# Kernel tuning notes

Measured on AMD Instinct MI355X. Metric: run time of the kernel, lower is better.

Reference implementation:

```python
import jax, jax.numpy as jnp
import numpy as np

EPS = 1e-5

def conv1x1(x, w, b):
    # x: [B,C,H,W], w: [O,C], b: [O]
    return jnp.einsum('bchw,oc->bohw', x, w) + b[None, :, None, None]

def bn_eval(x, g, b, m, v):
    scale = g / jnp.sqrt(v + EPS)
    return x * scale[None, :, None, None] + (b - m * scale)[None, :, None, None]

def setup_inputs() -> dict:
    key = jax.random.key(0)
    ks = jax.random.split(key, 32)
    B, Ch, Cl, H, W = 8, 256, 128, 64, 64
    r = Cl // 2
    red = 16  # CBAM channel-attention reduction
    s = 0.05
    n = lambda k, shape: jax.random.normal(k, shape, dtype=jnp.float32) * s
    inp = {
        'x': jax.random.normal(ks[0], (B, Ch, H, W), dtype=jnp.float32),
        'x0': jax.random.normal(ks[1], (B, Cl, H, W), dtype=jnp.float32),
        # CNL (flag=0)
        'cnl_g_w': n(ks[2], (Cl, Cl)), 'cnl_g_b': n(ks[3], (Cl,)),
        'cnl_theta_w': n(ks[4], (Cl, Ch)), 'cnl_theta_b': n(ks[5], (Cl,)),
        'cnl_phi_w': n(ks[6], (Cl, Cl)), 'cnl_phi_b': n(ks[7], (Cl,)),
        'cnl_W_w': n(ks[8], (Ch, Cl)), 'cnl_W_b': n(ks[9], (Ch,)),
        'cnl_bn_g': n(ks[10], (Ch,)), 'cnl_bn_b': n(ks[11], (Ch,)),
        'cnl_bn_m': n(ks[12], (Ch,)),
        'cnl_bn_v': jax.random.uniform(ks[13], (Ch,), dtype=jnp.float32) + 0.5,
        # PNL (reduc_ratio=2)
        'pnl_g_w': n(ks[14], (r, Cl)), 'pnl_g_b': n(ks[15], (r,)),
        'pnl_theta_w': n(ks[16], (r, Ch)), 'pnl_theta_b': n(ks[17], (r,)),
        'pnl_phi_w': n(ks[18], (r, Cl)), 'pnl_phi_b': n(ks[19], (r,)),
        'pnl_W_w': n(ks[20], (Ch, r)), 'pnl_W_b': n(ks[21], (Ch,)),
        'pnl_bn_g': n(ks[22], (Ch,)), 'pnl_bn_b': n(ks[23], (Ch,)),
        'pnl_bn_m': n(ks[24], (Ch,)),
        'pnl_bn_v': jax.random.uniform(ks[25], (Ch,), dtype=jnp.float32) + 0.5,
        # CBAM
        'ca_fc1_w': n(ks[26], (Ch // red, Ch)),
        'ca_fc2_w': n(ks[27], (Ch, Ch // red)),
        'sa_conv_w': n(ks[28], (1, 2, 7, 7)),
        'fusion_weight': jnp.float32(0.5),
    }
    return inp

def mdfo_forward(x, x0, cnl_g_w, cnl_g_b, cnl_theta_w, cnl_theta_b, cnl_phi_w, cnl_phi_b,
                 cnl_W_w, cnl_W_b, cnl_bn_g, cnl_bn_b, cnl_bn_m, cnl_bn_v,
                 pnl_g_w, pnl_g_b, pnl_theta_w, pnl_theta_b, pnl_phi_w, pnl_phi_b,
                 pnl_W_w, pnl_W_b, pnl_bn_g, pnl_bn_b, pnl_bn_m, pnl_bn_v,
                 ca_fc1_w, ca_fc2_w, sa_conv_w, fusion_weight):
    B, Ch, H, W = x.shape
    Cl = x0.shape[1]
    N = H * W
    # ---- CNL (flag=0): channel-space affinity [B, Cl, Cl] ----
    g_x = conv1x1(x0, cnl_g_w, cnl_g_b).reshape(B, Cl, N)
    th = conv1x1(x, cnl_theta_w, cnl_theta_b).reshape(B, Cl, N)
    ph = conv1x1(x0, cnl_phi_w, cnl_phi_b).reshape(B, Cl, N)
    att = jnp.einsum('bcn,bdn->bcd', th, ph) / Cl  # energy / energy.size(-1)
    y = jnp.einsum('bcd,bdn->bcn', att, g_x).reshape(B, Cl, H, W)
    z_cnl = bn_eval(conv1x1(y, cnl_W_w, cnl_W_b), cnl_bn_g, cnl_bn_b, cnl_bn_m, cnl_bn_v) + x
    # ---- PNL: pixel-space affinity [B, N/2, N/2] (faithful channel-folding reshape) ----
    r = Cl // 2
    M = N // 2
    g2 = conv1x1(x0, pnl_g_w, pnl_g_b).reshape(B, Cl, M).transpose(0, 2, 1)          # [B,M,Cl]
    t2 = conv1x1(z_cnl, pnl_theta_w, pnl_theta_b).reshape(B, Cl, M).transpose(0, 2, 1)
    p2 = conv1x1(x0, pnl_phi_w, pnl_phi_b).reshape(B, Cl, M)
    att2 = jnp.einsum('bnc,bcm->bnm', t2, p2) / M
    y2 = jnp.einsum('bnm,bmc->bnc', att2, g2).transpose(0, 2, 1).reshape(B, r, H, W)
    z_pnl = bn_eval(conv1x1(y2, pnl_W_w, pnl_W_b), pnl_bn_g, pnl_bn_b, pnl_bn_m, pnl_bn_v) + z_cnl
    # ---- CBAM: channel attention then spatial attention ----
    def mlp(v):
        return jnp.einsum('bh,oh->bo', jax.nn.relu(jnp.einsum('bc,hc->bh', v, ca_fc1_w)), ca_fc2_w)
    ca = jax.nn.sigmoid(mlp(z_pnl.mean(axis=(2, 3))) + mlp(z_pnl.max(axis=(2, 3))))
    xc = z_pnl * ca[:, :, None, None]
    sa_in = jnp.concatenate([xc.mean(axis=1, keepdims=True), xc.max(axis=1, keepdims=True)], axis=1)
    sa = jax.lax.conv_general_dilated(sa_in, sa_conv_w, (1, 1), ((3, 3), (3, 3)),
                                      dimension_numbers=('NCHW', 'OIHW', 'NCHW'))
    z_cbam = xc * jax.nn.sigmoid(sa)
    # ---- weighted fusion (dropout is identity in eval mode) ----
    return fusion_weight * z_cbam + (1.0 - fusion_weight) * x

def reference(x, x0, cnl_g_w, cnl_g_b, cnl_theta_w, cnl_theta_b, cnl_phi_w, cnl_phi_b,
              cnl_W_w, cnl_W_b, cnl_bn_g, cnl_bn_b, cnl_bn_m, cnl_bn_v,
              pnl_g_w, pnl_g_b, pnl_theta_w, pnl_theta_b, pnl_phi_w, pnl_phi_b,
              pnl_W_w, pnl_W_b, pnl_bn_g, pnl_bn_b, pnl_bn_m, pnl_bn_v,
              ca_fc1_w, ca_fc2_w, sa_conv_w, fusion_weight):
    return mdfo_forward(x, x0, cnl_g_w, cnl_g_b, cnl_theta_w, cnl_theta_b, cnl_phi_w, cnl_phi_b,
                        cnl_W_w, cnl_W_b, cnl_bn_g, cnl_bn_b, cnl_bn_m, cnl_bn_v,
                        pnl_g_w, pnl_g_b, pnl_theta_w, pnl_theta_b, pnl_phi_w, pnl_phi_b,
                        pnl_W_w, pnl_W_b, pnl_bn_g, pnl_bn_b, pnl_bn_m, pnl_bn_v,
                        ca_fc1_w, ca_fc2_w, sa_conv_w, fusion_weight)
```

## Files before the change

kernel.cpp:

```cpp
#include <hip/hip_runtime.h>
#include <math.h>

typedef unsigned short u16;
typedef unsigned int   u32;
typedef __bf16 bf16_8 __attribute__((ext_vector_type(8)));
typedef float  f32x4  __attribute__((ext_vector_type(4)));

constexpr int CH   = 256;
constexpr int NPIX = 4096;

__device__ __forceinline__ u16 f2bf(float f) {
    u32 u = __float_as_uint(f);
    u = (u + 0x7FFFu + ((u >> 16) & 1u)) >> 16;
    return (u16)u;
}
__device__ __forceinline__ float bf2f(u16 h) { return __uint_as_float((u32)h << 16); }
__device__ __forceinline__ u32 encF(float f) {
    u32 u = __float_as_uint(f);
    return u ^ (u32)(((int)u >> 31) | 0x80000000);
}
__device__ __forceinline__ float decF(u32 u) {
    return __uint_as_float((u >> 31) ? (u ^ 0x80000000u) : ~u);
}

struct GJob {
    const u16* A; const u16* B;
    u16* outB; float* outF; u32* maxOut;
    const float* bias; const float* bng; const float* bnb; const float* bnm;
    const float* bnv; const u16* resB;
    long long sA, sB, sC, sR;
    int lda, ldb, ldc, K, nSplit, mode, biasRow, gx, gy, nBlk;
};
struct GJobs { GJob j[4]; int n; };

template<int BN>
__global__ __launch_bounds__(256, 2)
void mfma_multi(GJobs jobs)
{
    constexpr int BM = 64, BK = 64;
    constexpr int WN = BN / 4;
    constexpr int NT = WN / 16;
    __shared__ __align__(16) u16 smem[BM * BK + BN * BK];
    u16* As = smem;
    u16* Bs = smem + BM * BK;
    u16* Ct = smem;
    float* sSum = (float*)&smem[BM * BN];
    u32*   sMax = (u32*)&smem[BM * BN + 512];

    int ji = 0, start = 0;
    {
        int bxx = blockIdx.x;
        while (ji + 1 < jobs.n && bxx >= start + jobs.j[ji].nBlk) {
            start += jobs.j[ji].nBlk; ++ji;
        }
    }
    const GJob J = jobs.j[ji];
    const int local = blockIdx.x - start;
    const int per = J.gx * J.gy;
    const int bz = local / per;
    const int r2 = local - bz * per;
    const int by = r2 / J.gx;
    const int bx2 = r2 - by * J.gx;
// ... 76 lines not shown
        int lc = wave * WN + nt * 16 + lm;
#pragma unroll
        for (int mt = 0; mt < 4; ++mt)
#pragma unroll
            for (int r = 0; r < 4; ++r)
                Ct[(mt * 16 + q * 4 + r) * BN + lc] = f2bf(acc[mt][nt][r]);
    }
    __syncthreads();

    constexpr int CPR = BN / 8;
    constexpr int RSTEP = 256 / CPR;
    constexpr int PT = BM / RSTEP;
    const int cc = (tid % CPR) * 8;
    const int lr0 = tid / CPR;

    float csc[8], csh[8], cbv[8];
    if (J.mode == 4 || J.mode == 5) {
#pragma unroll
        for (int j = 0; j < 8; ++j) {
            int C = nBase + cc + j;
            float sc = J.bng[C] * rsqrtf(J.bnv[C] + 1e-5f);
            csc[j] = sc;
            csh[j] = J.bnb[C] - J.bnm[C] * sc;
            cbv[j] = J.bias[C];
        }
    } else if (J.mode == 0 && J.bias && !J.biasRow) {
#pragma unroll
        for (int j = 0; j < 8; ++j) cbv[j] = J.bias[nBase + cc + j];
    } else {
#pragma unroll
        for (int j = 0; j < 8; ++j) cbv[j] = 0.f;
    }

    float tsum[8], tmax[8];
#pragma unroll
    for (int j = 0; j < 8; ++j) { tsum[j] = 0.f; tmax[j] = -1e30f; }

#pragma unroll
    for (int i = 0; i < PT; ++i) {
        int lr = lr0 + i * RSTEP;
        int R = mBase + lr;
        uint4 raw = *(const uint4*)&Ct[lr * BN + cc];
        u32 w[4] = {raw.x, raw.y, raw.z, raw.w};
        float v[8];
#pragma unroll
        for (int jj = 0; jj < 4; ++jj) {
            v[2 * jj]     = bf2f((u16)(w[jj] & 0xFFFFu));
            v[2 * jj + 1] = bf2f((u16)(w[jj] >> 16));
        }
        if (J.mode == 0) {
            float rb = (J.bias && J.biasRow) ? J.bias[R] : 0.f;
            u32 o[4];
#pragma unroll
            for (int jj = 0; jj < 4; ++jj) {
                u16 lo = f2bf(v[2 * jj] + cbv[2 * jj] + rb);
                u16 hi = f2bf(v[2 * jj + 1] + cbv[2 * jj + 1] + rb);
                o[jj] = (u32)lo | ((u32)hi << 16);
            }
            *(uint4*)&J.outB[(size_t)batch * J.sC + (size_t)R * J.ldc + nBase + cc] =
                make_uint4(o[0], o[1], o[2], o[3]);
        } else if (J.mode == 3) {
            u16 ev[4], od[4];
#pragma unroll
            for (int jj = 0; jj < 4; ++jj) {
                ev[jj] = f2bf(v[2 * jj]);
                od[jj] = f2bf(v[2 * jj + 1]);
            }
            int c0 = (cc >> 1);
            u32 e0 = (u32)ev[0] | ((u32)ev[1] << 16), e1 = (u32)ev[2] | ((u32)ev[3] << 16);
            u32 d0 = (u32)od[0] | ((u32)od[1] << 16), d1 = (u32)od[2] | ((u32)od[3] << 16);
            *(uint2*)&J.outB[(size_t)batch * J.sC + (size_t)R * 64 + c0] = make_uint2(e0, e1);
            *(uint2*)&J.outB[(size_t)batch * J.sC + (size_t)(R + 2048) * 64 + c0] = make_uint2(d0, d1);
        } else {
            size_t off = (size_t)batch * J.sC + (size_t)R * J.ldc + nBase + cc;
            uint4 rr = *(const uint4*)&J.resB[(size_t)batch * J.sR + (size_t)R * J.ldc + nBase + cc];
            u32 rw[4] = {rr.x, rr.y, rr.z, rr.w};
            u32 o[4];
#pragma unroll
            for (int jj = 0; jj < 4; ++jj) {
                float z0 = (v[2 * jj] + cbv[2 * jj]) * csc[2 * jj] + csh[2 * jj] +
                           bf2f((u16)(rw[jj] & 0xFFFFu));
                float z1 = (v[2 * jj + 1] + cbv[2 * jj + 1]) * csc[2 * jj + 1] +
                           csh[2 * jj + 1] + bf2f((u16)(rw[jj] >> 16));
                u16 lo = f2bf(z0), hi = f2bf(z1);
                o[jj] = (u32)lo | ((u32)hi << 16);
                tsum[2 * jj] += bf2f(lo); tsum[2 * jj + 1] += bf2f(hi);
                tmax[2 * jj] = fmaxf(tmax[2 * jj], bf2f(lo));
                tmax[2 * jj + 1] = fmaxf(tmax[2 * jj + 1], bf2f(hi));
            }
            *(uint4*)&J.outB[off] = make_uint4(o[0], o[1], o[2], o[3]);
        }
    }

    if (J.mode == 5) {
        sSum[tid] = 0.f; sMax[tid] = 0u;
        __syncthreads();
#pragma unroll
        for (int j = 0; j < 8; ++j) {
            atomicAdd(&sSum[cc + j], tsum[j]);
            atomicMax(&sMax[cc + j], encF(tmax[j]));
        }
        __syncthreads();
        atomicAdd(&J.outF[batch * CH + tid], sSum[tid]);
        atomicMax(&J.maxOut[batch * CH + tid], sMax[tid]);
    }
}

__global__ __launch_bounds__(256, 2)
void zcnl_t2(const u16* __restrict__ yTg, const u16* __restrict__ w_z,
             const u16* __restrict__ xTb, const u16* __restrict__ w_t2,
             u16* __restrict__ zb, u16* __restrict__ T2f,
             const float* __restrict__ bias,
             const float* __restrict__ bng, const float* __restrict__ bnb,
             const float* __restrict__ bnm, const float* __restrict__ bnv,
             const float* __restrict__ bias2)
{
    constexpr int BM = 64, BK = 64, BN = 256, WN = 64, NT = 4;
    constexpr int LDP = 264;
    __shared__ __align__(16) u16 smem[33792];
    u16* As = smem;
    u16* Bs = smem + 4096;
    u16* Ct = smem;
    u16* B2 = smem + 16896;

    const int batch = blockIdx.z;
    const int mBase = blockIdx.y * BM;
    const int tid = threadIdx.x;
    const int wave = tid >> 6, lane = tid & 63, lm = lane & 15, q = lane >> 4;
    const u16* Ab = yTg + (size_t)batch * 524288;

    f32x4 acc[4][NT];
#pragma unroll
    for (int i = 0; i < 4; ++i)
#pragma unroll
        for (int j = 0; j < NT; ++j) acc[i][j] = f32x4{0.f, 0.f, 0.f, 0.f};

    const int srow = tid >> 3, sc8 = tid & 7;
    for (int k0 = 0; k0 < 128; k0 += BK) {
        __syncthreads();
#pragma unroll
        for (int it = 0; it < 2; ++it) {
            int r = srow + it * 32;
            uint4 v = *(const uint4*)(Ab + (size_t)(mBase + r) * 128 + k0 + sc8 * 8);
            *(uint4*)&As[r * BK + ((sc8 ^ (r & 7)) * 8)] = v;
        }
#pragma unroll
        for (int it = 0; it < 8; ++it) {
            int r = srow + it * 32;
            uint4 v = *(const uint4*)(w_z + (size_t)r * 128 + k0 + sc8 * 8);
            *(uint4*)&Bs[r * BK + ((sc8 ^ (r & 7)) * 8)] = v;
        }
        __syncthreads();
#pragma unroll
        for (int ks = 0; ks < 2; ++ks) {
            bf16_8 af[4], bfr[NT];
#pragma unroll
            for (int mt = 0; mt < 4; ++mt) {
                int r = mt * 16 + lm;
                af[mt] = *(const bf16_8*)&As[r * BK + (((ks * 4 + q) ^ (lm & 7)) * 8)];
            }
#pragma unroll
            for (int nt = 0; nt < NT; ++nt) {
                int r = wave * WN + nt * 16 + lm;
                bfr[nt] = *(const bf16_8*)&Bs[r * BK + (((ks * 4 + q) ^ (lm & 7)) * 8)];
            }
#pragma unroll
            for (int mt = 0; mt < 4; ++mt)
#pragma unroll
                for (int nt = 0; nt < NT; ++nt)
                    acc[mt][nt] = __builtin_amdgcn_mfma_f32_16x16x32_bf16(
                        af[mt], bfr[nt], acc[mt][nt], 0, 0, 0);
        }
    }

    __syncthreads();
#pragma unroll
    for (int nt = 0; nt < NT; ++nt) {
        int lc = wave * WN + nt * 16 + lm;
#pragma unroll
        for (int mt = 0; mt < 4; ++mt)
#pragma unroll
            for (int r = 0; r < 4; ++r)
                Ct[(mt * 16 + q * 4 + r) * LDP + lc] = f2bf(acc[mt][nt][r]);
    }
#pragma unroll
    for (int i = 0; i < 8; ++i) {
        int id = tid + i * 256;
        int r = id >> 5, ch = id & 31;
        *(uint4*)&B2[r * LDP + ch * 8] = *(const uint4*)(w_t2 + r * 256 + ch * 8);
    }
    __syncthreads();

    const int cc = (tid & 31) * 8;
    const int lr0 = tid >> 5;
    float csc[8], csh[8], cbv[8];
#pragma unroll
    for (int j = 0; j < 8; ++j) {
        int C = cc + j;
        float sc = bng[C] * rsqrtf(bnv[C] + 1e-5f);
        csc[j] = sc;
        csh[j] = bnb[C] - bnm[C] * sc;
        cbv[j] = bias[C];
    }
#pragma unroll
    for (int i = 0; i < 8; ++i) {
        int lr = lr0 + i * 8;
        int R = mBase + lr;
        uint4 raw = *(const uint4*)&Ct[lr * LDP + cc];
        u32 w[4] = {raw.x, raw.y, raw.z, raw.w};
        uint4 rr = *(const uint4*)&xTb[(size_t)batch * 1048576 + (size_t)R * 256 + cc];
        u32 rw[4] = {rr.x, rr.y, rr.z, rr.w};
        u32 o[4];
#pragma unroll
        for (int jj = 0; jj < 4; ++jj) {
            float z0 = (bf2f((u16)(w[jj] & 0xFFFFu)) + cbv[2 * jj]) * csc[2 * jj] +
                       csh[2 * jj] + bf2f((u16)(rw[jj] & 0xFFFFu));
            float z1 = (bf2f((u16)(w[jj] >> 16)) + cbv[2 * jj + 1]) * csc[2 * jj + 1] +
                       csh[2 * jj + 1] + bf2f((u16)(rw[jj] >> 16));
            o[jj] = (u32)f2bf(z0) | ((u32)f2bf(z1) << 16);
        }
        *(uint4*)&zb[(size_t)batch * 1048576 + (size_t)R * 256 + cc] =
            make_uint4(o[0], o[1], o[2], o[3]);
        *(uint4*)&Ct[lr * LDP + cc] = make_uint4(o[0], o[1], o[2], o[3]);
    }
    __syncthreads();

    f32x4 acc2[4];
#pragma unroll
    for (int i = 0; i < 4; ++i) acc2[i] = f32x4{0.f, 0.f, 0.f, 0.f};
#pragma unroll
    for (int ks = 0; ks < 8; ++ks) {
        bf16_8 bf = *(const bf16_8*)&B2[(wave * 16 + lm) * LDP + ks * 32 + q * 8];
#pragma unroll
        for (int mt = 0; mt < 4; ++mt) {
            bf16_8 af = *(const bf16_8*)&Ct[(mt * 16 + lm) * LDP + ks * 32 + q * 8];
            acc2[mt] = __builtin_amdgcn_mfma_f32_16x16x32_bf16(af, bf, acc2[mt], 0, 0, 0);
        }
    }
    const int d = wave * 16 + lm;
    const float b2v = bias2[d];
#pragma unroll
    for (int mt = 0; mt < 4; ++mt)
#pragma unroll
        for (int r = 0; r < 4; ++r) {
            int pix = mBase + mt * 16 + q * 4 + r;
            T2f[(size_t)batch * 262144 + (size_t)(pix & 2047) * 128 + (pix >> 11) * 64 + d] =
                f2bf(acc2[mt][r] + b2v);
        }
}

__global__ __launch_bounds__(256)
void prep_tcast(const float* __restrict__ x, u16* __restrict__ xTb,
                const float* __restrict__ x0, u16* __restrict__ x0Tb,
                const float* w0, const float* w1, const float* w2, const float* w3,
                const float* w4, const float* w5, const float* w6, const float* w7,
                const float* pgb, const float* ppb,
                float* __restrict__ zr, u16* __restrict__ wsb, float* __restrict__ pb128)
{
    __shared__ u16 T[64][68];
    const int bx = blockIdx.x, tid = threadIdx.x;
    if (bx < 3072) {
        const int b = bx / 384, rem = bx % 384;
        const int by = rem / 64, nb = (rem % 64) * 64;
// ... 28 lines not shown
            if      (j < 32768)  v = w0[j];
            else if (j < 49152)  v = w1[j - 32768];
            else if (j < 65536)  v = w2[j - 49152];
            else if (j < 98304)  v = w3[j - 65536];
            else if (j < 106496) v = w4[j - 98304];
            else if (j < 114688) v = w5[j - 106496];
            else if (j < 131072) v = w6[j - 114688];
            else                 v = w7[j - 131072];
            wsb[j] = f2bf(v);
        }
        int k = i - 413696;
        if (k >= 0 && k < 128) pb128[k] = (k < 64) ? pgb[k] : ppb[k - 64];
    }
}

__global__ void cast2(const float* __restrict__ attF, u16* __restrict__ attb,
                      const float* __restrict__ SF, u16* __restrict__ Sb)
{
    int i = blockIdx.x * 256 + threadIdx.x;
    if (i < 131072) {
        attb[i] = f2bf(attF[i] * (1.f / 128.f));
    } else {
        int j = i - 131072;
        int dd = j & 127;
        int src = (j & ~127) + 2 * (dd & 63) + (dd >> 6);
        Sb[j] = f2bf(SF[src] * (1.f / 2048.f));
    }
}

__global__ __launch_bounds__(256)
void sa_ca(const u16* __restrict__ z, const float* __restrict__ meanS,
           const u32* __restrict__ maxU, const float* __restrict__ fc1,
           const float* __restrict__ fc2, float* __restrict__ ca,
           float* __restrict__ sain)
{
    const int b = blockIdx.y, tid = threadIdx.x;
    __shared__ float s_avg[CH], s_mx[CH], s_h[16], s_ca[CH];
    s_avg[tid] = meanS[b * CH + tid] * (1.f / NPIX);
    s_mx[tid]  = decF(maxU[b * CH + tid]);
    __syncthreads();
    if (tid < 16) {
        float ha = 0.f, hm = 0.f;
        for (int c = 0; c < CH; ++c) {
            float w = fc1[tid * CH + c];
// ... 79 lines not shown
            T[cl][n] = v * cav * s_sig[n];
        }
    }
    __syncthreads();
    {
        int nl = tid & 63, cq = tid >> 6;
#pragma unroll
        for (int i = 0; i < 16; ++i) {
            int c = cq * 16 + i;
            size_t o = (size_t)b * CH * NPIX + (size_t)(cb + c) * NPIX + nb + nl;
            out[o] = fw * T[c][nl] + (1.f - fw) * x[o];
        }
    }
}

static GJob mkjob(const u16* A, const u16* B, u16* outB, float* outF, u32* maxOut,
                  const float* bias, const float* bng, const float* bnb,
                  const float* bnm, const float* bnv, const u16* resB,
                  long long sA, long long sB, long long sC, long long sR,
                  int lda, int ldb, int ldc, int K, int nSplit, int mode,
                  int biasRow, int gx, int gy)
{
    GJob g;
    g.A = A; g.B = B; g.outB = outB; g.outF = outF; g.maxOut = maxOut;
    g.bias = bias; g.bng = bng; g.bnb = bnb; g.bnm = bnm; g.bnv = bnv; g.resB = resB;
    g.sA = sA; g.sB = sB; g.sC = sC; g.sR = sR;
    g.lda = lda; g.ldb = ldb; g.ldc = ldc; g.K = K; g.nSplit = nSplit;
    g.mode = mode; g.biasRow = biasRow; g.gx = gx; g.gy = gy;
    g.nBlk = gx * gy * 8 * nSplit;
    return g;
}

extern "C" void kernel_launch(void* const* d_in, const int* in_sizes, int n_in,
                              void* d_out, int out_size, void* d_ws, size_t ws_size,
                              hipStream_t stream)
{
    const float* x        = (const float*)d_in[0];
    const float* x0       = (const float*)d_in[1];
    const float* cnl_g_w  = (const float*)d_in[2];
    const float* cnl_g_b  = (const float*)d_in[3];
    const float* cnl_th_w = (const float*)d_in[4];
// ... 18 lines not shown
    const float* pnl_bn_b = (const float*)d_in[23];
    const float* pnl_bn_m = (const float*)d_in[24];
    const float* pnl_bn_v = (const float*)d_in[25];
    const float* ca_fc1   = (const float*)d_in[26];
    const float* ca_fc2   = (const float*)d_in[27];
    const float* sa_w     = (const float*)d_in[28];
    const float* fw       = (const float*)d_in[29];
    float* out = (float*)d_out;
    char* wsc  = (char*)d_ws;

    u16* xTb   = (u16*)(wsc + 0);
    u16* x0Tb  = (u16*)(wsc + 16777216);
    u16* thcn  = (u16*)(wsc + 25165824);
    u16* phcn  = (u16*)(wsc + 33554432);
    u16* gT    = (u16*)(wsc + 41943040);
    u16* yT    = (u16*)(wsc + 50331648);
    u16* zb    = (u16*)(wsc + 58720256);
    u16* g2p2  = (u16*)(wsc + 75497472);
    float* attF  = (float*)(wsc + 83886080);
    float* SF    = (float*)(wsc + 84410368);
    float* meanS = (float*)(wsc + 84934656);
    u32*   maxU  = (u32*)  (wsc + 84942848);
    u16* attb  = (u16*)(wsc + 84951040);
    u16* Sb    = (u16*)(wsc + 85213184);
    float* ca  = (float*)(wsc + 85475328);
    float* sain= (float*)(wsc + 85483520);
    u16* wsb   = (u16*)(wsc + 85745664);
    float* pb128 = (float*)(wsc + 86040576);
    u16* T2f   = phcn;
    u16* Ync   = phcn + 2097152;

    u16* w_th = wsb + 0;
    u16* w_ph = wsb + 32768;
    u16* w_g  = wsb + 49152;
    u16* w_z  = wsb + 65536;
    u16* w_gp = wsb + 98304;
    u16* w_t2 = wsb + 114688;
    u16* w_zp = wsb + 131072;

    const long long sX  = 1048576, sX0 = 524288, sCN = 524288, sAt = 16384;

    prep_tcast<<<dim3(4689), dim3(256), 0, stream>>>(x, xTb, x0, x0Tb,
        cnl_th_w, cnl_ph_w, cnl_g_w, cnl_W_w, pnl_g_w, pnl_ph_w, pnl_th_w, pnl_W_w,
        pnl_g_b, pnl_ph_b, attF, wsb, pb128);

    GJobs L1{}; L1.n = 4;
    L1.j[0] = mkjob(w_th, xTb, thcn, 0, 0, cnl_th_b, 0, 0, 0, 0, 0,
                    0, sX, sCN, 0, 256, 256, 4096, 256, 1, 0, 1, 32, 2);
    L1.j[1] = mkjob(w_ph, x0Tb, phcn, 0, 0, cnl_ph_b, 0, 0, 0, 0, 0,
                    0, sX0, sCN, 0, 128, 128, 4096, 128, 1, 0, 1, 32, 2);
    L1.j[2] = mkjob(x0Tb, w_g, gT, 0, 0, cnl_g_b, 0, 0, 0, 0, 0,
                    sX0, 0, sX0, 0, 128, 128, 128, 128, 1, 0, 0, 1, 64);
    L1.j[3] = mkjob(w_gp, x0Tb, g2p2, 0, 0, pb128, 0, 0, 0, 0, 0,
                    0, sX0, sCN, 0, 128, 128, 4096, 128, 1, 0, 1, 32, 2);
    mfma_multi<128><<<dim3(2048), dim3(256), 0, stream>>>(L1);

    GJobs SK{}; SK.n = 2;
    SK.j[0] = mkjob(thcn, phcn, 0, attF, 0, 0, 0, 0, 0, 0, 0,
                    sCN, sCN, sAt, 0, 4096, 4096, 128, 4096, 16, 1, 0, 1, 2);
    SK.j[1] = mkjob(g2p2, g2p2 + 262144, 0, SF, 0, 0, 0, 0, 0, 0, 0,
                    sCN, sCN, sAt, 0, 2048, 2048, 128, 2048, 8, 1, 0, 1, 2);
    mfma_multi<128><<<dim3(384), dim3(256), 0, stream>>>(SK);

    cast2<<<dim3(1024), dim3(256), 0, stream>>>(attF, attb, SF, Sb);

    GJobs JY{}; JY.n = 1;
    JY.j[0] = mkjob(gT, attb, yT, 0, 0, 0, 0, 0, 0, 0, 0,
                    sX0, sAt, sX0, 0, 128, 128, 128, 128, 1, 0, 0, 1, 64);
    mfma_multi<128><<<dim3(512), dim3(256), 0, stream>>>(JY);

    zcnl_t2<<<dim3(1, 64, 8), dim3(256), 0, stream>>>(yT, w_z, xTb, w_t2, zb, T2f,
        cnl_W_b, cnl_bn_g, cnl_bn_b, cnl_bn_m, cnl_bn_v, pnl_th_b);

    GJobs JG{}; JG.n = 1;
    JG.j[0] = mkjob(T2f, Sb, Ync, 0, 0, 0, 0, 0, 0, 0, 0,
                    262144, sAt, 262144, 0, 128, 128, 64, 128, 1, 3, 0, 1, 32);
    mfma_multi<128><<<dim3(256), dim3(256), 0, stream>>>(JG);

    GJobs JZ{}; JZ.n = 1;
    JZ.j[0] = mkjob(Ync, w_zp, zb, meanS, maxU, pnl_W_b,
                    pnl_bn_g, pnl_bn_b, pnl_bn_m, pnl_bn_v, zb,
                    262144, 0, sX, sX, 64, 64, 256, 64, 1, 5, 0, 1, 64);
    mfma_multi<256><<<dim3(512), dim3(256), 0, stream>>>(JZ);

    sa_ca<<<dim3(64, 8), dim3(256), 0, stream>>>(zb, meanS, maxU, ca_fc1, ca_fc2, ca, sain);
    fuse_conv<<<dim3(64, 4, 8), dim3(256), 0, stream>>>(zb, ca, sain, sa_w, x, fw, out);
}
```

Baseline: 261.7 us.

## Fuse attention-apply GEMMs into CNL and PNL chain kernels, drop cast pass

Replaces the separate cast2 kernel, the y = g·att GEMM, and the zcnl_t2 kernel with one fused y3 kernel. y3 loads the fp32 attention matrix, scales and casts it into shared memory, computes y, the W-projection with BN and residual, and the T2 projection without leaving the block. It also fuses the PNL Y = T2·S GEMM with the W_z projection, BN and channel sum/max reduction into a new p3 kernel. This removes several launches and the global round trips for attb, Sb, yT and Ync. In exchange each block redoes the attention matrix conversion, and the fused kernels use more shared memory and registers.

```diff
diff --git a/kernel.cpp b/kernel.cpp
--- a/kernel.cpp
+++ b/kernel.cpp
@@ -25,10 +25,9 @@
 
 struct GJob {
     const u16* A; const u16* B;
-    u16* outB; float* outF; u32* maxOut;
-    const float* bias; const float* bng; const float* bnb; const float* bnm;
-    const float* bnv; const u16* resB;
-    long long sA, sB, sC, sR;
+    u16* outB; float* outF;
+    const float* bias;
+    long long sA, sB, sC;
     int lda, ldb, ldc, K, nSplit, mode, biasRow, gx, gy, nBlk;
 };
 struct GJobs { GJob j[4]; int n; };
@@ -44,8 +43,6 @@
     u16* As = smem;
     u16* Bs = smem + BM * BK;
     u16* Ct = smem;
-    float* sSum = (float*)&smem[BM * BN];
-    u32*   sMax = (u32*)&smem[BM * BN + 512];
 
     int ji = 0, start = 0;
     {
@@ -152,27 +149,14 @@
     const int cc = (tid % CPR) * 8;
     const int lr0 = tid / CPR;
 
-    float csc[8], csh[8], cbv[8];
-    if (J.mode == 4 || J.mode == 5) {
-#pragma unroll
-        for (int j = 0; j < 8; ++j) {
-            int C = nBase + cc + j;
-            float sc = J.bng[C] * rsqrtf(J.bnv[C] + 1e-5f);
-            csc[j] = sc;
-            csh[j] = J.bnb[C] - J.bnm[C] * sc;
-            cbv[j] = J.bias[C];
-        }
-    } else if (J.mode == 0 && J.bias && !J.biasRow) {
+    float cbv[8];
+    if (J.bias && !J.biasRow) {
 #pragma unroll
         for (int j = 0; j < 8; ++j) cbv[j] = J.bias[nBase + cc + j];
     } else {
 #pragma unroll
         for (int j = 0; j < 8; ++j) cbv[j] = 0.f;
     }
-
-    float tsum[8], tmax[8];
-#pragma unroll
-    for (int j = 0; j < 8; ++j) { tsum[j] = 0.f; tmax[j] = -1e30f; }
 
 #pragma unroll
     for (int i = 0; i < PT; ++i) {
@@ -180,45 +164,399 @@
         int R = mBase + lr;
         uint4 raw = *(const uint4*)&Ct[lr * BN + cc];
         u32 w[4] = {raw.x, raw.y, raw.z, raw.w};
-        float v[8];
+        float rb = (J.bias && J.biasRow) ? J.bias[R] : 0.f;
+        u32 o[4];
 #pragma unroll
         for (int jj = 0; jj < 4; ++jj) {
-            v[2 * jj]     = bf2f((u16)(w[jj] & 0xFFFFu));
-            v[2 * jj + 1] = bf2f((u16)(w[jj] >> 16));
-        }
-        if (J.mode == 0) {
-            float rb = (J.bias && J.biasRow) ? J.bias[R] : 0.f;
+            u16 lo = f2bf(bf2f((u16)(w[jj] & 0xFFFFu)) + cbv[2 * jj] + rb);
+            u16 hi = f2bf(bf2f((u16)(w[jj] >> 16)) + cbv[2 * jj + 1] + rb);
+            o[jj] = (u32)lo | ((u32)hi << 16);
+        }
+        *(uint4*)&J.outB[(size_t)batch * J.sC + (size_t)R * J.ldc + nBase + cc] =
+            make_uint4(o[0], o[1], o[2], o[3]);
+    }
+}
+
+__global__ __launch_bounds__(256, 2)
+void y3(const u16* __restrict__ gT, const float* __restrict__ attF,
+        const u16* __restrict__ w_z, const u16* __restrict__ xTb,
+        const u16* __restrict__ w_t2,
+        u16* __restrict__ zb, u16* __restrict__ T2f,
+        const float* __restrict__ bias, const float* __restrict__ bng,
+        const float* __restrict__ bnb, const float* __restrict__ bnm,
+        const float* __restrict__ bnv, const float* __restrict__ bias2)
+{
+    __shared__ __align__(16) u16 smem[40960];
+    u16* sAtt = smem;
+    u16* yA   = smem + 16384;
+    u16* Bs   = smem + 24576;
+
+    const int bz = blockIdx.z, mBase = blockIdx.y * 64;
+    const int tid = threadIdx.x;
+    const int wave = tid >> 6, lane = tid & 63, lm = lane & 15, q = lane >> 4;
+    const int srow = tid >> 3, sc8 = tid & 7;
+
+    {
+        const float* src = attF + (size_t)bz * 16384;
+#pragma unroll
+        for (int i = 0; i < 8; ++i) {
+            int id = tid + i * 256;
+            int r = id >> 4, cg = id & 15;
+            int kc = cg >> 3, c8 = cg & 7;
+            const float* s = src + r * 128 + kc * 64 + c8 * 8;
             u32 o[4];
 #pragma unroll
-            for (int jj = 0; jj < 4; ++jj) {
-                u16 lo = f2bf(v[2 * jj] + cbv[2 * jj] + rb);
-                u16 hi = f2bf(v[2 * jj + 1] + cbv[2 * jj + 1] + rb);
-                o[jj] = (u32)lo | ((u32)hi << 16);
-            }
-            *(uint4*)&J.outB[(size_t)batch * J.sC + (size_t)R * J.ldc + nBase + cc] =
+            for (int j = 0; j < 4; ++j) {
+                u16 lo = f2bf(s[2 * j] * (1.f / 128.f));
+                u16 hi = f2bf(s[2 * j + 1] * (1.f / 128.f));
+                o[j] = (u32)lo | ((u32)hi << 16);
+            }
+            *(uint4*)&sAtt[kc * 8192 + r * 64 + ((c8 ^ (r & 7)) * 8)] =
                 make_uint4(o[0], o[1], o[2], o[3]);
-        } else if (J.mode == 3) {
-            u16 ev[4], od[4];
-#pragma unroll
-            for (int jj = 0; jj < 4; ++jj) {
-                ev[jj] = f2bf(v[2 * jj]);
-                od[jj] = f2bf(v[2 * jj + 1]);
-            }
-            int c0 = (cc >> 1);
-            u32 e0 = (u32)ev[0] | ((u32)ev[1] << 16), e1 = (u32)ev[2] | ((u32)ev[3] << 16);
-            u32 d0 = (u32)od[0] | ((u32)od[1] << 16), d1 = (u32)od[2] | ((u32)od[3] << 16);
-            *(uint2*)&J.outB[(size_t)batch * J.sC + (size_t)R * 64 + c0] = make_uint2(e0, e1);
-            *(uint2*)&J.outB[(size_t)batch * J.sC + (size_t)(R + 2048) * 64 + c0] = make_uint2(d0, d1);
-        } else {
-            size_t off = (size_t)batch * J.sC + (size_t)R * J.ldc + nBase + cc;
-            uint4 rr = *(const uint4*)&J.resB[(size_t)batch * J.sR + (size_t)R * J.ldc + nBase + cc];
+        }
+    }
+
+    f32x4 acc1[4][2];
+#pragma unroll
+    for (int i = 0; i < 4; ++i)
+#pragma unroll
+        for (int j = 0; j < 2; ++j) acc1[i][j] = f32x4{0.f, 0.f, 0.f, 0.f};
+    for (int kc = 0; kc < 2; ++kc) {
+        __syncthreads();
+#pragma unroll
+        for (int it = 0; it < 2; ++it) {
+            int r = srow + it * 32;
+            uint4 v = *(const uint4*)(gT + (size_t)bz * 524288 +
+                                      (size_t)(mBase + r) * 128 + kc * 64 + sc8 * 8);
+            *(uint4*)&yA[r * 64 + ((sc8 ^ (r & 7)) * 8)] = v;
+        }
+        __syncthreads();
+#pragma unroll
+        for (int ks = 0; ks < 2; ++ks) {
+            bf16_8 af[4], bfr[2];
+#pragma unroll
+            for (int mt = 0; mt < 4; ++mt) {
+                int m = mt * 16 + lm;
+                af[mt] = *(const bf16_8*)&yA[m * 64 + (((ks * 4 + q) ^ (m & 7)) * 8)];
+            }
+#pragma unroll
+            for (int nt = 0; nt < 2; ++nt) {
+                int rb = wave * 32 + nt * 16 + lm;
+                bfr[nt] = *(const bf16_8*)&sAtt[kc * 8192 + rb * 64 +
+                                                (((ks * 4 + q) ^ (rb & 7)) * 8)];
+            }
+#pragma unroll
+            for (int mt = 0; mt < 4; ++mt)
+#pragma unroll
+                for (int nt = 0; nt < 2; ++nt)
+                    acc1[mt][nt] = __builtin_amdgcn_mfma_f32_16x16x32_bf16(
+                        af[mt], bfr[nt], acc1[mt][nt], 0, 0, 0);
+        }
+    }
+    __syncthreads();
+#pragma unroll
+    for (int nt = 0; nt < 2; ++nt) {
+        int pcol = wave * 32 + nt * 16 + lm;
+        int kc = pcol >> 6, c = pcol & 63;
+#pragma unroll
+        for (int mt = 0; mt < 4; ++mt)
+#pragma unroll
+            for (int r = 0; r < 4; ++r) {
+                int prow = mt * 16 + q * 4 + r;
+                yA[kc * 4096 + prow * 64 + (((c >> 3) ^ (prow & 7)) * 8) + (c & 7)] =
+                    f2bf(acc1[mt][nt][r]);
+            }
+    }
+
+    f32x4 acc2[4][4];
+#pragma unroll
+    for (int i = 0; i < 4; ++i)
+#pragma unroll
+        for (int j = 0; j < 4; ++j) acc2[i][j] = f32x4{0.f, 0.f, 0.f, 0.f};
+    for (int kc = 0; kc < 2; ++kc) {
+        __syncthreads();
+#pragma unroll
+        for (int it = 0; it < 8; ++it) {
+            int r = srow + it * 32;
+            uint4 v = *(const uint4*)(w_z + (size_t)r * 128 + kc * 64 + sc8 * 8);
+            *(uint4*)&Bs[r * 64 + ((sc8 ^ (r & 7)) * 8)] = v;
+        }
+        __syncthreads();
+#pragma unroll
+        for (int ks = 0; ks < 2; ++ks) {
+            bf16_8 af[4], bfr[4];
+#pragma unroll
+            for (int mt = 0; mt < 4; ++mt) {
+                int m = mt * 16 + lm;
+                af[mt] = *(const bf16_8*)&yA[kc * 4096 + m * 64 +
+                                             (((ks * 4 + q) ^ (m & 7)) * 8)];
+            }
+#pragma unroll
+            for (int nt = 0; nt < 4; ++nt) {
+                int rb = wave * 64 + nt * 16 + lm;
+                bfr[nt] = *(const bf16_8*)&Bs[rb * 64 + (((ks * 4 + q) ^ (rb & 7)) * 8)];
+            }
+#pragma unroll
+            for (int mt = 0; mt < 4; ++mt)
+#pragma unroll
+                for (int nt = 0; nt < 4; ++nt)
+                    acc2[mt][nt] = __builtin_amdgcn_mfma_f32_16x16x32_bf16(
+                        af[mt], bfr[nt], acc2[mt][nt], 0, 0, 0);
+        }
+    }
+#pragma unroll
+    for (int nt = 0; nt < 4; ++nt) {
+        int pcol = wave * 64 + nt * 16 + lm;
+        int kc = pcol >> 6, c = pcol & 63;
+#pragma unroll
+        for (int mt = 0; mt < 4; ++mt)
+#pragma unroll
+            for (int r = 0; r < 4; ++r) {
+                int prow = mt * 16 + q * 4 + r;
+                sAtt[kc * 4096 + prow * 64 + (((c >> 3) ^ (prow & 7)) * 8) + (c & 7)] =
+                    f2bf(acc2[mt][nt][r]);
+            }
+    }
+    __syncthreads();
+
+    {
+        const int cc = (tid & 31) * 8, lr0 = tid >> 5;
+        float csc[8], csh[8], cbv[8];
+#pragma unroll
+        for (int j = 0; j < 8; ++j) {
+            int C = cc + j;
+            float sc = bng[C] * rsqrtf(bnv[C] + 1e-5f);
+            csc[j] = sc;
+            csh[j] = bnb[C] - bnm[C] * sc;
+            cbv[j] = bias[C];
+        }
+        int kcz = cc >> 6, c8z = (cc & 63) >> 3;
+#pragma unroll
+        for (int i = 0; i < 8; ++i) {
+            int lr = lr0 + i * 8;
+            int R = mBase + lr;
+            int a = kcz * 4096 + lr * 64 + ((c8z ^ (lr & 7)) * 8);
+            uint4 raw = *(const uint4*)&sAtt[a];
+            u32 w[4] = {raw.x, raw.y, raw.z, raw.w};
+            uint4 rr = *(const uint4*)&xTb[(size_t)bz * 1048576 + (size_t)R * 256 + cc];
             u32 rw[4] = {rr.x, rr.y, rr.z, rr.w};
             u32 o[4];
 #pragma unroll
             for (int jj = 0; jj < 4; ++jj) {
-                float z0 = (v[2 * jj] + cbv[2 * jj]) * csc[2 * jj] + csh[2 * jj] +
-                           bf2f((u16)(rw[jj] & 0xFFFFu));
-                float z1 = (v[2 * jj + 1] + cbv[2 * jj + 1]) * csc[2 * jj + 1] +
+                float z0 = (bf2f((u16)(w[jj] & 0xFFFFu)) + cbv[2 * jj]) * csc[2 * jj] +
+                           csh[2 * jj] + bf2f((u16)(rw[jj] & 0xFFFFu));
+                float z1 = (bf2f((u16)(w[jj] >> 16)) + cbv[2 * jj + 1]) * csc[2 * jj + 1] +
+                           csh[2 * jj + 1] + bf2f((u16)(rw[jj] >> 16));
+                o[jj] = (u32)f2bf(z0) | ((u32)f2bf(z1) << 16);
+            }
+            *(uint4*)&zb[(size_t)bz * 1048576 + (size_t)R * 256 + cc] =
+                make_uint4(o[0], o[1], o[2], o[3]);
+            *(uint4*)&sAtt[a] = make_uint4(o[0], o[1], o[2], o[3]);
+        }
+    }
+#pragma unroll
+    for (int i = 0; i < 8; ++i) {
+        int id = tid + i * 256;
+        int r = id >> 5, cg = id & 31;
+        int kc = cg >> 3, c8 = cg & 7;
+        uint4 v = *(const uint4*)(w_t2 + r * 256 + kc * 64 + c8 * 8);
+        *(uint4*)&Bs[kc * 4096 + r * 64 + ((c8 ^ (r & 7)) * 8)] = v;
+    }
+    __syncthreads();
+
+    f32x4 acc3[4];
+#pragma unroll
+    for (int i = 0; i < 4; ++i) acc3[i] = f32x4{0.f, 0.f, 0.f, 0.f};
+#pragma unroll
+    for (int kc = 0; kc < 4; ++kc)
+#pragma unroll
+        for (int ks = 0; ks < 2; ++ks) {
+            int rb = wave * 16 + lm;
+            bf16_8 bf = *(const bf16_8*)&Bs[kc * 4096 + rb * 64 +
+                                            (((ks * 4 + q) ^ (rb & 7)) * 8)];
+#pragma unroll
+            for (int mt = 0; mt < 4; ++mt) {
+                int m = mt * 16 + lm;
+                bf16_8 af = *(const bf16_8*)&sAtt[kc * 4096 + m * 64 +
+                                                  (((ks * 4 + q) ^ (m & 7)) * 8)];
+                acc3[mt] = __builtin_amdgcn_mfma_f32_16x16x32_bf16(af, bf, acc3[mt], 0, 0, 0);
+            }
+        }
+    const int d = wave * 16 + lm;
+    const float b2 = bias2[d];
+#pragma unroll
+    for (int mt = 0; mt < 4; ++mt)
+#pragma unroll
+        for (int r = 0; r < 4; ++r) {
+            int pix = mBase + mt * 16 + q * 4 + r;
+            T2f[(size_t)bz * 262144 + (size_t)(pix & 2047) * 128 + (pix >> 11) * 64 + d] =
+                f2bf(acc3[mt][r] + b2);
+        }
+}
+
+__global__ __launch_bounds__(256, 2)
+void p3(const u16* __restrict__ T2f, const float* __restrict__ SF,
+        const u16* __restrict__ w_zp, u16* __restrict__ zb,
+        float* __restrict__ meanS, u32* __restrict__ maxU,
+        const float* __restrict__ bias, const float* __restrict__ bng,
+        const float* __restrict__ bnb, const float* __restrict__ bnm,
+        const float* __restrict__ bnv)
+{
+    __shared__ __align__(16) u16 smem[26624];
+    u16* sS = smem;
+    u16* yA = smem + 16896;
+    float* sSum = (float*)&smem[25600];
+    u32*   sMax = (u32*)&smem[26112];
+
+    const int bz = blockIdx.z, mBase2 = blockIdx.y * 64;
+    const int tid = threadIdx.x;
+    const int wave = tid >> 6, lane = tid & 63, lm = lane & 15, q = lane >> 4;
+    const int srow = tid >> 3, sc8 = tid & 7;
+
+    {
+        const float* src = SF + (size_t)bz * 16384;
+#pragma unroll
+        for (int i = 0; i < 8; ++i) {
+            int id = tid + i * 256;
+            int r = id >> 4, cg = id & 15;
+            int kc = cg >> 3, c8 = cg & 7;
+            int k0 = kc * 64 + c8 * 8;
+            u32 o[4];
+#pragma unroll
+            for (int j = 0; j < 4; ++j) {
+                int ka = k0 + 2 * j, kb = ka + 1;
+                float va = src[r * 128 + 2 * (ka & 63) + (ka >> 6)] * (1.f / 2048.f);
+                float vb = src[r * 128 + 2 * (kb & 63) + (kb >> 6)] * (1.f / 2048.f);
+                o[j] = (u32)f2bf(va) | ((u32)f2bf(vb) << 16);
+            }
+            *(uint4*)&sS[kc * 8192 + r * 64 + ((c8 ^ (r & 7)) * 8)] =
+                make_uint4(o[0], o[1], o[2], o[3]);
+        }
+    }
+
+    f32x4 acc1[4][2];
+#pragma unroll
+    for (int i = 0; i < 4; ++i)
+#pragma unroll
+        for (int j = 0; j < 2; ++j) acc1[i][j] = f32x4{0.f, 0.f, 0.f, 0.f};
+    for (int kc = 0; kc < 2; ++kc) {
+        __syncthreads();
+#pragma unroll
+        for (int it = 0; it < 2; ++it) {
+            int r = srow + it * 32;
+            uint4 v = *(const uint4*)(T2f + (size_t)bz * 262144 +
+                                      (size_t)(mBase2 + r) * 128 + kc * 64 + sc8 * 8);
+            *(uint4*)&yA[r * 64 + ((sc8 ^ (r & 7)) * 8)] = v;
+        }
+        __syncthreads();
+#pragma unroll
+        for (int ks = 0; ks < 2; ++ks) {
+            bf16_8 af[4], bfr[2];
+#pragma unroll
+            for (int mt = 0; mt < 4; ++mt) {
+                int m = mt * 16 + lm;
+                af[mt] = *(const bf16_8*)&yA[m * 64 + (((ks * 4 + q) ^ (m & 7)) * 8)];
+            }
+#pragma unroll
+            for (int nt = 0; nt < 2; ++nt) {
+                int rb = wave * 32 + nt * 16 + lm;
+                bfr[nt] = *(const bf16_8*)&sS[kc * 8192 + rb * 64 +
+                                              (((ks * 4 + q) ^ (rb & 7)) * 8)];
+            }
+#pragma unroll
+            for (int mt = 0; mt < 4; ++mt)
+#pragma unroll
+                for (int nt = 0; nt < 2; ++nt)
+                    acc1[mt][nt] = __builtin_amdgcn_mfma_f32_16x16x32_bf16(
+                        af[mt], bfr[nt], acc1[mt][nt], 0, 0, 0);
+        }
+    }
+    __syncthreads();
+#pragma unroll
+    for (int nt = 0; nt < 2; ++nt) {
+        int pcol = wave * 32 + nt * 16 + lm;
+        int half = pcol & 1, ch = pcol >> 1;
+#pragma unroll
+        for (int mt = 0; mt < 4; ++mt)
+#pragma unroll
+            for (int r = 0; r < 4; ++r) {
+                int prow = mt * 16 + q * 4 + r;
+                yA[(half * 64 + prow) * 68 + ch] = f2bf(acc1[mt][nt][r]);
+            }
+    }
+#pragma unroll
+    for (int it = 0; it < 8; ++it) {
+        int r = srow + it * 32;
+        uint4 v = *(const uint4*)(w_zp + (size_t)r * 64 + sc8 * 8);
+        *(uint4*)&sS[r * 64 + ((sc8 ^ (r & 7)) * 8)] = v;
+    }
+    __syncthreads();
+
+    f32x4 acc2[8][4];
+#pragma unroll
+    for (int i = 0; i < 8; ++i)
+#pragma unroll
+        for (int j = 0; j < 4; ++j) acc2[i][j] = f32x4{0.f, 0.f, 0.f, 0.f};
+#pragma unroll
+    for (int ks = 0; ks < 2; ++ks) {
+        bf16_8 bfr[4];
+#pragma unroll
+        for (int nt = 0; nt < 4; ++nt) {
+            int rb = wave * 64 + nt * 16 + lm;
+            bfr[nt] = *(const bf16_8*)&sS[rb * 64 + (((ks * 4 + q) ^ (rb & 7)) * 8)];
+        }
+#pragma unroll
+        for (int mt = 0; mt < 8; ++mt) {
+            int m = mt * 16 + lm;
+            bf16_8 af = *(const bf16_8*)&yA[m * 68 + ks * 32 + q * 8];
+#pragma unroll
+            for (int nt = 0; nt < 4; ++nt)
+                acc2[mt][nt] = __builtin_amdgcn_mfma_f32_16x16x32_bf16(
+                    af, bfr[nt], acc2[mt][nt], 0, 0, 0);
+        }
+    }
+
+    const int cc = (tid & 31) * 8, lr0 = tid >> 5;
+    float csc[8], csh[8], cbv[8], tsum[8], tmax[8];
+#pragma unroll
+    for (int j = 0; j < 8; ++j) {
+        int C = cc + j;
+        float sc = bng[C] * rsqrtf(bnv[C] + 1e-5f);
+        csc[j] = sc;
+        csh[j] = bnb[C] - bnm[C] * sc;
+        cbv[j] = bias[C];
+        tsum[j] = 0.f; tmax[j] = -1e30f;
+    }
+#pragma unroll
+    for (int h = 0; h < 2; ++h) {
+        __syncthreads();
+#pragma unroll
+        for (int nt = 0; nt < 4; ++nt) {
+            int pcol = wave * 64 + nt * 16 + lm;
+#pragma unroll
+            for (int mt = 0; mt < 4; ++mt)
+#pragma unroll
+                for (int r = 0; r < 4; ++r) {
+                    int prow = mt * 16 + q * 4 + r;
+                    sS[prow * 264 + pcol] = f2bf(acc2[h * 4 + mt][nt][r]);
+                }
+        }
+        __syncthreads();
+#pragma unroll
+        for (int i = 0; i < 8; ++i) {
+            int lr = lr0 + i * 8;
+            int pix = h * 2048 + mBase2 + lr;
+            uint4 raw = *(const uint4*)&sS[lr * 264 + cc];
+            u32 w[4] = {raw.x, raw.y, raw.z, raw.w};
+            size_t off = (size_t)bz * 1048576 + (size_t)pix * 256 + cc;
+            uint4 rr = *(const uint4*)&zb[off];
+            u32 rw[4] = {rr.x, rr.y, rr.z, rr.w};
+            u32 o[4];
+#pragma unroll
+            for (int jj = 0; jj < 4; ++jj) {
+                float z0 = (bf2f((u16)(w[jj] & 0xFFFFu)) + cbv[2 * jj]) * csc[2 * jj] +
+                           csh[2 * jj] + bf2f((u16)(rw[jj] & 0xFFFFu));
+                float z1 = (bf2f((u16)(w[jj] >> 16)) + cbv[2 * jj + 1]) * csc[2 * jj + 1] +
                            csh[2 * jj + 1] + bf2f((u16)(rw[jj] >> 16));
                 u16 lo = f2bf(z0), hi = f2bf(z1);
                 o[jj] = (u32)lo | ((u32)hi << 16);
@@ -226,165 +564,20 @@
                 tmax[2 * jj] = fmaxf(tmax[2 * jj], bf2f(lo));
                 tmax[2 * jj + 1] = fmaxf(tmax[2 * jj + 1], bf2f(hi));
             }
-            *(uint4*)&J.outB[off] = make_uint4(o[0], o[1], o[2], o[3]);
-        }
-    }
-
-    if (J.mode == 5) {
-        sSum[tid] = 0.f; sMax[tid] = 0u;
-        __syncthreads();
-#pragma unroll
-        for (int j = 0; j < 8; ++j) {
-            atomicAdd(&sSum[cc + j], tsum[j]);
-            atomicMax(&sMax[cc + j], encF(tmax[j]));
-        }
-        __syncthreads();
-        atomicAdd(&J.outF[batch * CH + tid], sSum[tid]);
-        atomicMax(&J.maxOut[batch * CH + tid], sMax[tid]);
-    }
-}
-
-__global__ __launch_bounds__(256, 2)
-void zcnl_t2(const u16* __restrict__ yTg, const u16* __restrict__ w_z,
-             const u16* __restrict__ xTb, const u16* __restrict__ w_t2,
-             u16* __restrict__ zb, u16* __restrict__ T2f,
-             const float* __restrict__ bias,
-             const float* __restrict__ bng, const float* __restrict__ bnb,
-             const float* __restrict__ bnm, const float* __restrict__ bnv,
-             const float* __restrict__ bias2)
-{
-    constexpr int BM = 64, BK = 64, BN = 256, WN = 64, NT = 4;
-    constexpr int LDP = 264;
-    __shared__ __align__(16) u16 smem[33792];
-    u16* As = smem;
-    u16* Bs = smem + 4096;
-    u16* Ct = smem;
-    u16* B2 = smem + 16896;
-
-    const int batch = blockIdx.z;
-    const int mBase = blockIdx.y * BM;
-    const int tid = threadIdx.x;
-    const int wave = tid >> 6, lane = tid & 63, lm = lane & 15, q = lane >> 4;
-    const u16* Ab = yTg + (size_t)batch * 524288;
-
-    f32x4 acc[4][NT];
-#pragma unroll
-    for (int i = 0; i < 4; ++i)
-#pragma unroll
-        for (int j = 0; j < NT; ++j) acc[i][j] = f32x4{0.f, 0.f, 0.f, 0.f};
-
-    const int srow = tid >> 3, sc8 = tid & 7;
-    for (int k0 = 0; k0 < 128; k0 += BK) {
-        __syncthreads();
-#pragma unroll
-        for (int it = 0; it < 2; ++it) {
-            int r = srow + it * 32;
-            uint4 v = *(const uint4*)(Ab + (size_t)(mBase + r) * 128 + k0 + sc8 * 8);
-            *(uint4*)&As[r * BK + ((sc8 ^ (r & 7)) * 8)] = v;
-        }
-#pragma unroll
-        for (int it = 0; it < 8; ++it) {
-            int r = srow + it * 32;
-            uint4 v = *(const uint4*)(w_z + (size_t)r * 128 + k0 + sc8 * 8);
-            *(uint4*)&Bs[r * BK + ((sc8 ^ (r & 7)) * 8)] = v;
-        }
-        __syncthreads();
-#pragma unroll
-        for (int ks = 0; ks < 2; ++ks) {
-            bf16_8 af[4], bfr[NT];
-#pragma unroll
-            for (int mt = 0; mt < 4; ++mt) {
-                int r = mt * 16 + lm;
-                af[mt] = *(const bf16_8*)&As[r * BK + (((ks * 4 + q) ^ (lm & 7)) * 8)];
-            }
-#pragma unroll
-            for (int nt = 0; nt < NT; ++nt) {
-                int r = wave * WN + nt * 16 + lm;
-                bfr[nt] = *(const bf16_8*)&Bs[r * BK + (((ks * 4 + q) ^ (lm & 7)) * 8)];
-            }
-#pragma unroll
-            for (int mt = 0; mt < 4; ++mt)
-#pragma unroll
-                for (int nt = 0; nt < NT; ++nt)
-                    acc[mt][nt] = __builtin_amdgcn_mfma_f32_16x16x32_bf16(
-                        af[mt], bfr[nt], acc[mt][nt], 0, 0, 0);
-        }
-    }
-
-    __syncthreads();
-#pragma unroll
-    for (int nt = 0; nt < NT; ++nt) {
-        int lc = wave * WN + nt * 16 + lm;
-#pragma unroll
-        for (int mt = 0; mt < 4; ++mt)
-#pragma unroll
-            for (int r = 0; r < 4; ++r)
-                Ct[(mt * 16 + q * 4 + r) * LDP + lc] = f2bf(acc[mt][nt][r]);
-    }
-#pragma unroll
-    for (int i = 0; i < 8; ++i) {
-        int id = tid + i * 256;
-        int r = id >> 5, ch = id & 31;
-        *(uint4*)&B2[r * LDP + ch * 8] = *(const uint4*)(w_t2 + r * 256 + ch * 8);
-    }
-    __syncthreads();
-
-    const int cc = (tid & 31) * 8;
-    const int lr0 = tid >> 5;
-    float csc[8], csh[8], cbv[8];
+            *(uint4*)&zb[off] = make_uint4(o[0], o[1], o[2], o[3]);
+        }
+    }
+    __syncthreads();
+    sSum[tid] = 0.f; sMax[tid] = 0u;
+    __syncthreads();
 #pragma unroll
     for (int j = 0; j < 8; ++j) {
-        int C = cc + j;
-        float sc = bng[C] * rsqrtf(bnv[C] + 1e-5f);
-        csc[j] = sc;
-        csh[j] = bnb[C] - bnm[C] * sc;
-        cbv[j] = bias[C];
-    }
-#pragma unroll
-    for (int i = 0; i < 8; ++i) {
-        int lr = lr0 + i * 8;
-        int R = mBase + lr;
-        uint4 raw = *(const uint4*)&Ct[lr * LDP + cc];
-        u32 w[4] = {raw.x, raw.y, raw.z, raw.w};
-        uint4 rr = *(const uint4*)&xTb[(size_t)batch * 1048576 + (size_t)R * 256 + cc];
-        u32 rw[4] = {rr.x, rr.y, rr.z, rr.w};
-        u32 o[4];
-#pragma unroll
-        for (int jj = 0; jj < 4; ++jj) {
-            float z0 = (bf2f((u16)(w[jj] & 0xFFFFu)) + cbv[2 * jj]) * csc[2 * jj] +
-                       csh[2 * jj] + bf2f((u16)(rw[jj] & 0xFFFFu));
-            float z1 = (bf2f((u16)(w[jj] >> 16)) + cbv[2 * jj + 1]) * csc[2 * jj + 1] +
-                       csh[2 * jj + 1] + bf2f((u16)(rw[jj] >> 16));
-            o[jj] = (u32)f2bf(z0) | ((u32)f2bf(z1) << 16);
-        }
-        *(uint4*)&zb[(size_t)batch * 1048576 + (size_t)R * 256 + cc] =
-            make_uint4(o[0], o[1], o[2], o[3]);
-        *(uint4*)&Ct[lr * LDP + cc] = make_uint4(o[0], o[1], o[2], o[3]);
-    }
-    __syncthreads();
-
-    f32x4 acc2[4];
-#pragma unroll
-    for (int i = 0; i < 4; ++i) acc2[i] = f32x4{0.f, 0.f, 0.f, 0.f};
-#pragma unroll
-    for (int ks = 0; ks < 8; ++ks) {
-        bf16_8 bf = *(const bf16_8*)&B2[(wave * 16 + lm) * LDP + ks * 32 + q * 8];
-#pragma unroll
-        for (int mt = 0; mt < 4; ++mt) {
-            bf16_8 af = *(const bf16_8*)&Ct[(mt * 16 + lm) * LDP + ks * 32 + q * 8];
-            acc2[mt] = __builtin_amdgcn_mfma_f32_16x16x32_bf16(af, bf, acc2[mt], 0, 0, 0);
-        }
-    }
-    const int d = wave * 16 + lm;
-    const float b2v = bias2[d];
-#pragma unroll
-    for (int mt = 0; mt < 4; ++mt)
-#pragma unroll
-        for (int r = 0; r < 4; ++r) {
-            int pix = mBase + mt * 16 + q * 4 + r;
-            T2f[(size_t)batch * 262144 + (size_t)(pix & 2047) * 128 + (pix >> 11) * 64 + d] =
-                f2bf(acc2[mt][r] + b2v);
-        }
+        atomicAdd(&sSum[cc + j], tsum[j]);
+        atomicMax(&sMax[cc + j], encF(tmax[j]));
+    }
+    __syncthreads();
+    atomicAdd(&meanS[bz * CH + tid], sSum[tid]);
+    atomicMax(&maxU[bz * CH + tid], sMax[tid]);
 }
 
 __global__ __launch_bounds__(256)
@@ -443,20 +636,6 @@
     }
 }
 
-__global__ void cast2(const float* __restrict__ attF, u16* __restrict__ attb,
-                      const float* __restrict__ SF, u16* __restrict__ Sb)
-{
-    int i = blockIdx.x * 256 + threadIdx.x;
-    if (i < 131072) {
-        attb[i] = f2bf(attF[i] * (1.f / 128.f));
-    } else {
-        int j = i - 131072;
-        int dd = j & 127;
-        int src = (j & ~127) + 2 * (dd & 63) + (dd >> 6);
-        Sb[j] = f2bf(SF[src] * (1.f / 2048.f));
-    }
-}
-
 __global__ __launch_bounds__(256)
 void sa_ca(const u16* __restrict__ z, const float* __restrict__ meanS,
            const u32* __restrict__ maxU, const float* __restrict__ fc1,
@@ -566,17 +745,15 @@
     }
 }
 
-static GJob mkjob(const u16* A, const u16* B, u16* outB, float* outF, u32* maxOut,
-                  const float* bias, const float* bng, const float* bnb,
-                  const float* bnm, const float* bnv, const u16* resB,
-                  long long sA, long long sB, long long sC, long long sR,
+static GJob mkjob(const u16* A, const u16* B, u16* outB, float* outF,
+                  const float* bias,
+                  long long sA, long long sB, long long sC,
                   int lda, int ldb, int ldc, int K, int nSplit, int mode,
                   int biasRow, int gx, int gy)
 {
     GJob g;
-    g.A = A; g.B = B; g.outB = outB; g.outF = outF; g.maxOut = maxOut;
-    g.bias = bias; g.bng = bng; g.bnb = bnb; g.bnm = bnm; g.bnv = bnv; g.resB = resB;
-    g.sA = sA; g.sB = sB; g.sC = sC; g.sR = sR;
+    g.A = A; g.B = B; g.outB = outB; g.outF = outF; g.bias = bias;
+    g.sA = sA; g.sB = sB; g.sC = sC;
     g.lda = lda; g.ldb = ldb; g.ldc = ldc; g.K = K; g.nSplit = nSplit;
     g.mode = mode; g.biasRow = biasRow; g.gx = gx; g.gy = gy;
     g.nBlk = gx * gy * 8 * nSplit;
@@ -625,21 +802,17 @@
     u16* thcn  = (u16*)(wsc + 25165824);
     u16* phcn  = (u16*)(wsc + 33554432);
     u16* gT    = (u16*)(wsc + 41943040);
-    u16* yT    = (u16*)(wsc + 50331648);
     u16* zb    = (u16*)(wsc + 58720256);
     u16* g2p2  = (u16*)(wsc + 75497472);
     float* attF  = (float*)(wsc + 83886080);
     float* SF    = (float*)(wsc + 84410368);
     float* meanS = (float*)(wsc + 84934656);
     u32*   maxU  = (u32*)  (wsc + 84942848);
-    u16* attb  = (u16*)(wsc + 84951040);
-    u16* Sb    = (u16*)(wsc + 85213184);
     float* ca  = (float*)(wsc + 85475328);
     float* sain= (float*)(wsc + 85483520);
     u16* wsb   = (u16*)(wsc + 85745664);
     float* pb128 = (float*)(wsc + 86040576);
     u16* T2f   = phcn;
-    u16* Ync   = phcn + 2097152;
 
     u16* w_th = wsb + 0;
     u16* w_ph = wsb + 32768;
@@ -649,50 +822,36 @@
     u16* w_t2 = wsb + 114688;
     u16* w_zp = wsb + 131072;
 
-    const long long sX  = 1048576, sX0 = 524288, sCN = 524288, sAt = 16384;
+    const long long sX0 = 524288, sCN = 524288, sAt = 16384;
+    const long long sX  = 1048576;
 
     prep_tcast<<<dim3(4689), dim3(256), 0, stream>>>(x, xTb, x0, x0Tb,
         cnl_th_w, cnl_ph_w, cnl_g_w, cnl_W_w, pnl_g_w, pnl_ph_w, pnl_th_w, pnl_W_w,
         pnl_g_b, pnl_ph_b, attF, wsb, pb128);
 
     GJobs L1{}; L1.n = 4;
-    L1.j[0] = mkjob(w_th, xTb, thcn, 0, 0, cnl_th_b, 0, 0, 0, 0, 0,
-                    0, sX, sCN, 0, 256, 256, 4096, 256, 1, 0, 1, 32, 2);
-    L1.j[1] = mkjob(w_ph, x0Tb, phcn, 0, 0, cnl_ph_b, 0, 0, 0, 0, 0,
-                    0, sX0, sCN, 0, 128, 128, 4096, 128, 1, 0, 1, 32, 2);
-    L1.j[2] = mkjob(x0Tb, w_g, gT, 0, 0, cnl_g_b, 0, 0, 0, 0, 0,
-                    sX0, 0, sX0, 0, 128, 128, 128, 128, 1, 0, 0, 1, 64);
-    L1.j[3] = mkjob(w_gp, x0Tb, g2p2, 0, 0, pb128, 0, 0, 0, 0, 0,
-                    0, sX0, sCN, 0, 128, 128, 4096, 128, 1, 0, 1, 32, 2);
+    L1.j[0] = mkjob(w_th, xTb, thcn, 0, cnl_th_b, 0, sX, sCN,
+                    256, 256, 4096, 256, 1, 0, 1, 32, 2);
+    L1.j[1] = mkjob(w_ph, x0Tb, phcn, 0, cnl_ph_b, 0, sX0, sCN,
+                    128, 128, 4096, 128, 1, 0, 1, 32, 2);
+    L1.j[2] = mkjob(x0Tb, w_g, gT, 0, cnl_g_b, sX0, 0, sX0,
+                    128, 128, 128, 128, 1, 0, 0, 1, 64);
+    L1.j[3] = mkjob(w_gp, x0Tb, g2p2, 0, pb128, 0, sX0, sCN,
+                    128, 128, 4096, 128, 1, 0, 1, 32, 2);
     mfma_multi<128><<<dim3(2048), dim3(256), 0, stream>>>(L1);
 
     GJobs SK{}; SK.n = 2;
-    SK.j[0] = mkjob(thcn, phcn, 0, attF, 0, 0, 0, 0, 0, 0, 0,
-                    sCN, sCN, sAt, 0, 4096, 4096, 128, 4096, 16, 1, 0, 1, 2);
-    SK.j[1] = mkjob(g2p2, g2p2 + 262144, 0, SF, 0, 0, 0, 0, 0, 0, 0,
-                    sCN, sCN, sAt, 0, 2048, 2048, 128, 2048, 8, 1, 0, 1, 2);
+    SK.j[0] = mkjob(thcn, phcn, 0, attF, 0, sCN, sCN, sAt,
+                    4096, 4096, 128, 4096, 16, 1, 0, 1, 2);
+    SK.j[1] = mkjob(g2p2, g2p2 + 262144, 0, SF, 0, sCN, sCN, sAt,
+                    2048, 2048, 128, 2048, 8, 1, 0, 1, 2);
     mfma_multi<128><<<dim3(384), dim3(256), 0, stream>>>(SK);
 
-    cast2<<<dim3(1024), dim3(256), 0, stream>>>(attF, attb, SF, Sb);
-
-    GJobs JY{}; JY.n = 1;
-    JY.j[0] = mkjob(gT, attb, yT, 0, 0, 0, 0, 0, 0, 0, 0,
-                    sX0, sAt, sX0, 0, 128, 128, 128, 128, 1, 0, 0, 1, 64);
-    mfma_multi<128><<<dim3(512), dim3(256), 0, stream>>>(JY);
-
-    zcnl_t2<<<dim3(1, 64, 8), dim3(256), 0, stream>>>(yT, w_z, xTb, w_t2, zb, T2f,
+    y3<<<dim3(1, 64, 8), dim3(256), 0, stream>>>(gT, attF, w_z, xTb, w_t2, zb, T2f,
         cnl_W_b, cnl_bn_g, cnl_bn_b, cnl_bn_m, cnl_bn_v, pnl_th_b);
 
-    GJobs JG{}; JG.n = 1;
-    JG.j[0] = mkjob(T2f, Sb, Ync, 0, 0, 0, 0, 0, 0, 0, 0,
-                    262144, sAt, 262144, 0, 128, 128, 64, 128, 1, 3, 0, 1, 32);
-    mfma_multi<128><<<dim3(256), dim3(256), 0, stream>>>(JG);
-
-    GJobs JZ{}; JZ.n = 1;
-    JZ.j[0] = mkjob(Ync, w_zp, zb, meanS, maxU, pnl_W_b,
-                    pnl_bn_g, pnl_bn_b, pnl_bn_m, pnl_bn_v, zb,
-                    262144, 0, sX, sX, 64, 64, 256, 64, 1, 5, 0, 1, 64);
-    mfma_multi<256><<<dim3(512), dim3(256), 0, stream>>>(JZ);
+    p3<<<dim3(1, 32, 8), dim3(256), 0, stream>>>(T2f, SF, w_zp, zb, meanS, maxU,
+        pnl_W_b, pnl_bn_g, pnl_bn_b, pnl_bn_m, pnl_bn_v);
 
     sa_ca<<<dim3(64, 8), dim3(256), 0, stream>>>(zb, meanS, maxU, ca_fc1, ca_fc2, ca, sain);
     fuse_conv<<<dim3(64, 4, 8), dim3(256), 0, stream>>>(zb, ca, sain, sa_w, x, fw, out);
```

Measured after the change: 245.5 us. 6.2% less time.
